# Kernel tuning notes

Hardware: AMD Instinct MI355X
Metric: run time of the kernel (lower is better)

## Reference

```python
import jax, jax.numpy as jnp
import numpy as np

BS, QLEN, DIM, NH = 2, 2048, 1024, 16
HD = DIM // NH


def setup_inputs() -> dict:
    key = jax.random.key(0)
    ks = jax.random.split(key, 6)
    std = 0.02
    return {
        "x": jax.random.normal(ks[0], (BS, QLEN, DIM), dtype=jnp.float32),
        "mask": jnp.ones((BS, QLEN), dtype=jnp.float32),
        "Wq": jax.random.normal(ks[1], (DIM, DIM), dtype=jnp.float32) * std,
        "bq": jnp.zeros((DIM,), dtype=jnp.float32),
        "Wk": jax.random.normal(ks[2], (DIM, DIM), dtype=jnp.float32) * std,
        "bk": jnp.zeros((DIM,), dtype=jnp.float32),
        "Wv": jax.random.normal(ks[3], (DIM, DIM), dtype=jnp.float32) * std,
        "bv": jnp.zeros((DIM,), dtype=jnp.float32),
        "Wo": jax.random.normal(ks[4], (DIM, DIM), dtype=jnp.float32) * std,
        "bo": jnp.zeros((DIM,), dtype=jnp.float32),
    }


def reference(x, mask, Wq, bq, Wk, bk, Wv, bv, Wo, bo):
    bs, qlen, dim = x.shape
    # project and split heads: [bs, nh, len, hd]
    def split_heads(t):
        return t.reshape(bs, -1, NH, HD).transpose(0, 2, 1, 3)

    q = split_heads(x @ Wq + bq) / jnp.sqrt(jnp.float32(HD))
    k = split_heads(x @ Wk + bk)
    v = split_heads(x @ Wv + bv)

    scores = jnp.einsum("bhqd,bhkd->bhqk", q, k)  # [bs, nh, qlen, klen]
    m = mask.reshape(bs, 1, 1, -1)  # 2D mask -> broadcast over heads and q
    scores = scores - 1e30 * (1.0 - m)
    weights = jax.nn.softmax(scores, axis=-1)
    # dropout p=0.0 at inference -> no-op; head_mask is None
    context = jnp.einsum("bhqk,bhkd->bhqd", weights, v)
    context = context.transpose(0, 2, 1, 3).reshape(bs, qlen, NH * HD)
    return context @ Wo + bo
```

## Files before the change

kernel.cpp:

```cpp
#include <hip/hip_runtime.h>
#include <stdint.h>

#define BSZ  2
#define SEQ  2048
#define DIM  1024
#define NHD  16
#define HD   64
#define MTOT (BSZ*SEQ)

using short8  = __attribute__((ext_vector_type(8))) short;
using floatx4 = __attribute__((ext_vector_type(4))) float;

#define QSCALE 0.18033688011112042f
#define BIGM   1.44e30f

__device__ __forceinline__ unsigned short f2bf(float f) {
    unsigned int u = __float_as_uint(f);
    u += 0x7fffu + ((u >> 16) & 1u);
    return (unsigned short)(u >> 16);
}
__device__ __forceinline__ unsigned int pk2r(float a, float b) {
    unsigned int ua = __float_as_uint(a) + 0x8000u;
    unsigned int ub = __float_as_uint(b) + 0x8000u;
    return __builtin_amdgcn_perm(ub, ua, 0x07060302);
}

__device__ __forceinline__ void gll16(const void* g, const void* lds) {
    unsigned int loff = (unsigned int)(unsigned long long)lds;
    __builtin_amdgcn_global_load_lds(
        (const __attribute__((address_space(1))) unsigned int*)g,
        (__attribute__((address_space(3))) unsigned int*)loff, 16, 0, 0);
}

__global__ __launch_bounds__(256)
void conv_x(const float* __restrict__ X, unsigned short* __restrict__ Xbf) {
    size_t i = ((size_t)blockIdx.x * 256 + threadIdx.x) * 8;
    float4 a = *(const float4*)(X + i);
    float4 b = *(const float4*)(X + i + 4);
    uint4 u = {pk2r(a.x, a.y), pk2r(a.z, a.w), pk2r(b.x, b.y), pk2r(b.z, b.w)};
    *(uint4*)(Xbf + i) = u;
}

__global__ __launch_bounds__(256)
void conv_wt(const float* __restrict__ Wq, const float* __restrict__ Wk,
             const float* __restrict__ Wv, const float* __restrict__ Wo,
             unsigned short* __restrict__ Wt3, unsigned short* __restrict__ Wto)
{
    __shared__ float tile[64 * 65];
    const int z = blockIdx.z;
    const float* W = (z == 0) ? Wq : (z == 1) ? Wk : (z == 2) ? Wv : Wo;
    unsigned short* out = (z < 3) ? (Wt3 + (size_t)z * DIM * DIM) : Wto;
    const int k0 = blockIdx.x * 64, n0 = blockIdx.y * 64;
    const int t = threadIdx.x;
    const int r = t >> 2, c0 = (t & 3) * 16;
#pragma unroll
    for (int j = 0; j < 4; ++j) {
        float4 v = *(const float4*)&W[(size_t)(k0 + r) * DIM + n0 + c0 + j * 4];
        tile[r * 65 + c0 + j * 4 + 0] = v.x;
        tile[r * 65 + c0 + j * 4 + 1] = v.y;
        tile[r * 65 + c0 + j * 4 + 2] = v.z;
        tile[r * 65 + c0 + j * 4 + 3] = v.w;
    }
    __syncthreads();
    unsigned int p[8];
#pragma unroll
    for (int j = 0; j < 8; ++j)
        p[j] = pk2r(tile[(c0 + 2 * j) * 65 + r], tile[(c0 + 2 * j + 1) * 65 + r]);
    uint4 u0 = {p[0], p[1], p[2], p[3]}, u1 = {p[4], p[5], p[6], p[7]};
    unsigned short* dst = out + (size_t)(n0 + r) * DIM + k0 + c0;
    *(uint4*)dst = u0;
    *(uint4*)(dst + 8) = u1;
}

__global__ __launch_bounds__(256)
void qkv_gemm(const unsigned short* __restrict__ Xbf,
              const unsigned short* __restrict__ Wt3,
              const float* __restrict__ bq, const float* __restrict__ bk,
              const float* __restrict__ bv,
              unsigned short* __restrict__ Qb,
              unsigned short* __restrict__ Kb,
              unsigned short* __restrict__ VbT)
{
    __shared__ unsigned short As[128 * 32];
    __shared__ unsigned short Bs[128 * 32];

    const int t = threadIdx.x, w = t >> 6, lane = t & 63;
    const int lm = lane & 15, grp = lane >> 4;
    const int wm = w >> 1, wn = w & 1;
    const int m0 = blockIdx.x * 128;
    const int mat = blockIdx.y >> 3;
    const int n0 = (blockIdx.y & 7) * 128;
    const unsigned short* Bg = Wt3 + (size_t)mat * DIM * DIM;

    const int lr = lane >> 2, lc = (lane & 3) * 8;

    floatx4 acc[4][4];
#pragma unroll
    for (int i = 0; i < 4; ++i)
#pragma unroll
        for (int j = 0; j < 4; ++j) acc[i][j] = (floatx4){0.f, 0.f, 0.f, 0.f};

    for (int kt = 0; kt < DIM / 32; ++kt) {
        const int k0 = kt * 32;
        const int r0 = w * 16;
        gll16(Xbf + (size_t)(m0 + r0 + lr) * DIM + k0 + lc,      &As[r0 * 32]);
        gll16(Xbf + (size_t)(m0 + 64 + r0 + lr) * DIM + k0 + lc, &As[(64 + r0) * 32]);
        gll16(Bg  + (size_t)(n0 + r0 + lr) * DIM + k0 + lc,      &Bs[r0 * 32]);
        gll16(Bg  + (size_t)(n0 + 64 + r0 + lr) * DIM + k0 + lc, &Bs[(64 + r0) * 32]);
        __syncthreads();
        short8 af[4], bf[4];
#pragma unroll
        for (int mt = 0; mt < 4; ++mt)
            af[mt] = *(const short8*)&As[(wm * 64 + mt * 16 + lm) * 32 + grp * 8];
#pragma unroll
        for (int nt = 0; nt < 4; ++nt)
            bf[nt] = *(const short8*)&Bs[(wn * 64 + nt * 16 + lm) * 32 + grp * 8];
#pragma unroll
        for (int mt = 0; mt < 4; ++mt)
#pragma unroll
            for (int nt = 0; nt < 4; ++nt)
                acc[mt][nt] = __builtin_amdgcn_mfma_f32_16x16x32_bf16(af[mt], bf[nt], acc[mt][nt], 0, 0, 0);
        __syncthreads();
    }

    if (mat == 2) {
#pragma unroll
        for (int nt = 0; nt < 4; ++nt) {
            const int c = n0 + wn * 64 + nt * 16 + lm;
            const float bb = bv[c];
            const int h = c >> 6, d = c & 63;
#pragma unroll
            for (int mt = 0; mt < 4; ++mt) {
                const int r = m0 + wm * 64 + mt * 16 + grp * 4;
                const int b = r >> 11, s = r & 2047;
                const int si = s & 63, sb = s & ~63;
                const int cg = si >> 4, g = (si >> 2) & 3;
                const int unit = (((cg & 1) << 2) | g) ^ (d & 7);
                const int sph = sb + unit * 8 + ((cg >> 1) << 2);
                uint2 pv;
                pv.x = pk2r(acc[mt][nt][0] + bb, acc[mt][nt][1] + bb);
                pv.y = pk2r(acc[mt][nt][2] + bb, acc[mt][nt][3] + bb);
                *(uint2*)&VbT[(((size_t)(b * NHD + h)) * HD + d) * SEQ + sph] = pv;
            }
        }
    } else if (mat == 1) {
#pragma unroll
        for (int nt = 0; nt < 4; ++nt) {
            const int c = n0 + wn * 64 + nt * 16 + lm;
            const float bb = bk[c];
            const int h = c >> 6, d = c & 63;
#pragma unroll
            for (int mt = 0; mt < 4; ++mt)
#pragma unroll
                for (int reg = 0; reg < 4; ++reg) {
                    const int r = m0 + wm * 64 + mt * 16 + grp * 4 + reg;
                    const int b = r >> 11, s = r & 2047;
                    const int dphys = (((d >> 3) ^ (s & 7)) << 3) | (d & 7);
                    Kb[(((size_t)(b * NHD + h)) * SEQ + s) * HD + dphys] =
                        f2bf(acc[mt][nt][reg] + bb);
                }
        }
    } else {
#pragma unroll
        for (int nt = 0; nt < 4; ++nt) {
            const int c = n0 + wn * 64 + nt * 16 + lm;
            const float bb = bq[c];
            const int h = c >> 6, d = c & 63;
#pragma unroll
            for (int mt = 0; mt < 4; ++mt)
#pragma unroll
                for (int reg = 0; reg < 4; ++reg) {
                    const int r = m0 + wm * 64 + mt * 16 + grp * 4 + reg;
                    const int b = r >> 11, s = r & 2047;
                    Qb[(((size_t)(b * NHD + h)) * SEQ + s) * HD + d] =
                        f2bf((acc[mt][nt][reg] + bb) * QSCALE);
                }
        }
    }
}

__global__ __launch_bounds__(256, 4)
void attn(const unsigned short* __restrict__ Qb,
          const unsigned short* __restrict__ Kb,
          const unsigned short* __restrict__ VbT,
          const float* __restrict__ mask,
          unsigned short* __restrict__ Cb)
{
    __shared__ unsigned short Kt[2][64 * 64];
    __shared__ unsigned short Vt[2][64 * 64];
    __shared__ float Msk[SEQ];

    const int t = threadIdx.x, w = t >> 6, lane = t & 63;
    const int lm = lane & 15, grp = lane >> 4;
    const int x7 = lm & 7;
    const int bh = blockIdx.y, b = bh >> 4, h = bh & 15;
    const int q0 = blockIdx.x * 64;

    short8 qf[2];
    {
        const unsigned short* qrow = Qb + ((size_t)bh * SEQ + q0 + w * 16 + lm) * HD;
        qf[0] = *(const short8*)(qrow + grp * 8);
        qf[1] = *(const short8*)(qrow + 32 + grp * 8);
    }

    {
        const float* mb = mask + b * SEQ;
        const int i = t * 8;
        float4 a = *(const float4*)(mb + i);
        float4 c = *(const float4*)(mb + i + 4);
        float4 ra = {__builtin_fmaf(a.x, BIGM, -BIGM), __builtin_fmaf(a.y, BIGM, -BIGM),
                     __builtin_fmaf(a.z, BIGM, -BIGM), __builtin_fmaf(a.w, BIGM, -BIGM)};
        float4 rc = {__builtin_fmaf(c.x, BIGM, -BIGM), __builtin_fmaf(c.y, BIGM, -BIGM),
                     __builtin_fmaf(c.z, BIGM, -BIGM), __builtin_fmaf(c.w, BIGM, -BIGM)};
        *(float4*)&Msk[i]     = ra;
        *(float4*)&Msk[i + 4] = rc;
    }

    floatx4 oacc[4];
#pragma unroll
    for (int i = 0; i < 4; ++i) oacc[i] = (floatx4){0.f, 0.f, 0.f, 0.f};
    float lpart = 0.f;

    const unsigned short* Kg = Kb + (size_t)bh * SEQ * HD;
    const unsigned short* Vg = VbT + (size_t)bh * HD * SEQ;
    const int srow = lane >> 3, scol = (lane & 7) * 8;

    gll16(Kg + (size_t)(w * 16 + srow) * HD + scol,      &Kt[0][(w * 16) * 64]);
    gll16(Kg + (size_t)(w * 16 + 8 + srow) * HD + scol,  &Kt[0][(w * 16 + 8) * 64]);
    gll16(Vg + (size_t)(w * 16 + srow) * SEQ + scol,     &Vt[0][(w * 16) * 64]);
    gll16(Vg + (size_t)(w * 16 + 8 + srow) * SEQ + scol, &Vt[0][(w * 16 + 8) * 64]);

#pragma unroll 1
    for (int kt = 0; kt < SEQ / 64; ++kt) {
        const int cur = kt & 1;
        const int kb = kt * 64;
        __syncthreads();
        if (kt + 1 < SEQ / 64) {
            const int nxt = cur ^ 1, kn = (kt + 1) * 64;
            gll16(Kg + (size_t)(kn + w * 16 + srow) * HD + scol,      &Kt[nxt][(w * 16) * 64]);
            gll16(Kg + (size_t)(kn + w * 16 + 8 + srow) * HD + scol,  &Kt[nxt][(w * 16 + 8) * 64]);
            gll16(Vg + (size_t)(w * 16 + srow) * SEQ + kn + scol,     &Vt[nxt][(w * 16) * 64]);
            gll16(Vg + (size_t)(w * 16 + 8 + srow) * SEQ + kn + scol, &Vt[nxt][(w * 16 + 8) * 64]);
        }

        floatx4 sv[4];
#pragma unroll
        for (int cg = 0; cg < 4; ++cg) {
            short8 a0 = *(const short8*)&Kt[cur][(cg * 16 + lm) * 64 + ((grp    ) ^ x7) * 8];
            short8 a1 = *(const short8*)&Kt[cur][(cg * 16 + lm) * 64 + ((4 + grp) ^ x7) * 8];
            floatx4 s = (floatx4){0.f, 0.f, 0.f, 0.f};
            s = __builtin_amdgcn_mfma_f32_16x16x32_bf16(a0, qf[0], s, 0, 0, 0);
            s = __builtin_amdgcn_mfma_f32_16x16x32_bf16(a1, qf[1], s, 0, 0, 0);
            sv[cg] = s;
        }

        short8 vf[4][2];
#pragma unroll
        for (int dg = 0; dg < 4; ++dg) {
            vf[dg][0] = *(const short8*)&Vt[cur][(dg * 16 + lm) * 64 + ((grp    ) ^ x7) * 8];
            vf[dg][1] = *(const short8*)&Vt[cur][(dg * 16 + lm) * 64 + ((4 + grp) ^ x7) * 8];
        }

        float p[4][4];
#pragma unroll
        for (int cg = 0; cg < 4; ++cg) {
            float4 md = *(const float4*)&Msk[kb + cg * 16 + grp * 4];
            p[cg][0] = __builtin_exp2f(sv[cg][0] + md.x);
            p[cg][1] = __builtin_exp2f(sv[cg][1] + md.y);
            p[cg][2] = __builtin_exp2f(sv[cg][2] + md.z);
            p[cg][3] = __builtin_exp2f(sv[cg][3] + md.w);
            lpart += (p[cg][0] + p[cg][1]) + (p[cg][2] + p[cg][3]);
        }

        uint4 u0, u1;
        u0.x = pk2r(p[0][0], p[0][1]); u0.y = pk2r(p[0][2], p[0][3]);
        u0.z = pk2r(p[2][0], p[2][1]); u0.w = pk2r(p[2][2], p[2][3]);
        u1.x = pk2r(p[1][0], p[1][1]); u1.y = pk2r(p[1][2], p[1][3]);
        u1.z = pk2r(p[3][0], p[3][1]); u1.w = pk2r(p[3][2], p[3][3]);
        short8 ap0 = *(const short8*)&u0;
        short8 ap1 = *(const short8*)&u1;

#pragma unroll
        for (int dg = 0; dg < 4; ++dg) {
            oacc[dg] = __builtin_amdgcn_mfma_f32_16x16x32_bf16(ap0, vf[dg][0], oacc[dg], 0, 0, 0);
            oacc[dg] = __builtin_amdgcn_mfma_f32_16x16x32_bf16(ap1, vf[dg][1], oacc[dg], 0, 0, 0);
        }
    }

    lpart += __shfl_xor(lpart, 16);
    lpart += __shfl_xor(lpart, 32);
    const float linv = (lpart > 0.f) ? 1.0f / lpart : 0.f;
    float inv[4];
#pragma unroll
    for (int r = 0; r < 4; ++r) inv[r] = __shfl(linv, grp * 4 + r);
#pragma unroll
    for (int dg = 0; dg < 4; ++dg)
#pragma unroll
        for (int r = 0; r < 4; ++r) {
            const int s = q0 + w * 16 + grp * 4 + r;
            Cb[((size_t)(b * SEQ + s)) * DIM + h * HD + dg * 16 + lm] =
                f2bf(oacc[dg][r] * inv[r]);
        }
}

__global__ __launch_bounds__(256)
void out_gemm(const unsigned short* __restrict__ Cb,
              const unsigned short* __restrict__ Wto,
              const float* __restrict__ bo,
              float* __restrict__ out)
{
    __shared__ unsigned short As[128 * 32];
    __shared__ unsigned short Bs[64 * 32];

    const int t = threadIdx.x, w = t >> 6, lane = t & 63;
    const int lm = lane & 15, grp = lane >> 4;
    const int m0 = blockIdx.x * 128;
    const int n0 = blockIdx.y * 64;

    const int lr = lane >> 2, lc = (lane & 3) * 8;

    floatx4 acc[2][4];
#pragma unroll
    for (int i = 0; i < 2; ++i)
#pragma unroll
        for (int j = 0; j < 4; ++j) acc[i][j] = (floatx4){0.f, 0.f, 0.f, 0.f};

    for (int kt = 0; kt < DIM / 32; ++kt) {
        const int k0 = kt * 32;
        const int r0 = w * 16;
        gll16(Cb  + (size_t)(m0 + r0 + lr) * DIM + k0 + lc,      &As[r0 * 32]);
        gll16(Cb  + (size_t)(m0 + 64 + r0 + lr) * DIM + k0 + lc, &As[(64 + r0) * 32]);
        gll16(Wto + (size_t)(n0 + r0 + lr) * DIM + k0 + lc,      &Bs[r0 * 32]);
        __syncthreads();
        short8 af[2], bf[4];
#pragma unroll
        for (int mt = 0; mt < 2; ++mt)
            af[mt] = *(const short8*)&As[(w * 32 + mt * 16 + lm) * 32 + grp * 8];
#pragma unroll
        for (int nt = 0; nt < 4; ++nt)
            bf[nt] = *(const short8*)&Bs[(nt * 16 + lm) * 32 + grp * 8];
#pragma unroll
        for (int mt = 0; mt < 2; ++mt)
#pragma unroll
            for (int nt = 0; nt < 4; ++nt)
                acc[mt][nt] = __builtin_amdgcn_mfma_f32_16x16x32_bf16(af[mt], bf[nt], acc[mt][nt], 0, 0, 0);
        __syncthreads();
    }

#pragma unroll
    for (int nt = 0; nt < 4; ++nt) {
        const int c = n0 + nt * 16 + lm;
        const float bb = bo[c];
#pragma unroll
        for (int mt = 0; mt < 2; ++mt)
#pragma unroll
            for (int reg = 0; reg < 4; ++reg) {
                const int r = m0 + w * 32 + mt * 16 + grp * 4 + reg;
                out[(size_t)r * DIM + c] = acc[mt][nt][reg] + bb;
            }
    }
}

extern "C" void kernel_launch(void* const* d_in, const int* in_sizes, int n_in,
                              void* d_out, int out_size, void* d_ws, size_t ws_size,
                              hipStream_t stream)
{
    const float* x    = (const float*)d_in[0];
    const float* mask = (const float*)d_in[1];
    const float* Wq   = (const float*)d_in[2];
    const float* bq   = (const float*)d_in[3];
    const float* Wk   = (const float*)d_in[4];
    const float* bk   = (const float*)d_in[5];
    const float* Wv   = (const float*)d_in[6];
    const float* bv   = (const float*)d_in[7];
    const float* Wo   = (const float*)d_in[8];
    const float* bo   = (const float*)d_in[9];
    float* out = (float*)d_out;

    const size_t M1 = (size_t)DIM * DIM;
    unsigned short* Qb  = (unsigned short*)d_ws;
    unsigned short* Kb  = Qb  + 4 * M1;
    unsigned short* VbT = Kb  + 4 * M1;
    unsigned short* Cb  = VbT + 4 * M1;
    unsigned short* Xbf = Cb  + 4 * M1;
    unsigned short* Wt3 = Xbf + 4 * M1;
    unsigned short* Wto = Wt3 + 3 * M1;

    conv_x <<<dim3((MTOT * DIM) / 2048), 256, 0, stream>>>(x, Xbf);
    conv_wt<<<dim3(16, 16, 4), 256, 0, stream>>>(Wq, Wk, Wv, Wo, Wt3, Wto);
    qkv_gemm<<<dim3(MTOT / 128, 24), 256, 0, stream>>>(Xbf, Wt3, bq, bk, bv, Qb, Kb, VbT);
    attn<<<dim3(SEQ / 64, BSZ * NHD), 256, 0, stream>>>(Qb, Kb, VbT, mask, Cb);
    out_gemm<<<dim3(MTOT / 128, DIM / 64), 256, 0, stream>>>(Cb, Wto, bo, out);
}
```

Before: 218.1 us.

## Double-buffer GEMM tiles, swap MFMA operands for vector stores, precompute mask penalty

```diff
diff --git a/kernel.cpp b/kernel.cpp
--- a/kernel.cpp
+++ b/kernel.cpp
@@ -13,6 +13,7 @@
 
 #define QSCALE 0.18033688011112042f
 #define BIGM   1.44e30f
+#define NXB    ((MTOT * DIM) / 2048)
 
 __device__ __forceinline__ unsigned short f2bf(float f) {
     unsigned int u = __float_as_uint(f);
@@ -33,7 +34,22 @@
 }
 
 __global__ __launch_bounds__(256)
-void conv_x(const float* __restrict__ X, unsigned short* __restrict__ Xbf) {
+void conv_x(const float* __restrict__ X, unsigned short* __restrict__ Xbf,
+            const float* __restrict__ mask, float* __restrict__ Pen) {
+    if (blockIdx.x >= NXB) {
+        const int bb = blockIdx.x - NXB;
+        const int i = threadIdx.x * 8;
+        const float* mb = mask + bb * SEQ;
+        float4 a = *(const float4*)(mb + i);
+        float4 c = *(const float4*)(mb + i + 4);
+        float4 ra = {__builtin_fmaf(a.x, BIGM, -BIGM), __builtin_fmaf(a.y, BIGM, -BIGM),
+                     __builtin_fmaf(a.z, BIGM, -BIGM), __builtin_fmaf(a.w, BIGM, -BIGM)};
+        float4 rc = {__builtin_fmaf(c.x, BIGM, -BIGM), __builtin_fmaf(c.y, BIGM, -BIGM),
+                     __builtin_fmaf(c.z, BIGM, -BIGM), __builtin_fmaf(c.w, BIGM, -BIGM)};
+        *(float4*)&Pen[bb * SEQ + i]     = ra;
+        *(float4*)&Pen[bb * SEQ + i + 4] = rc;
+        return;
+    }
     size_t i = ((size_t)blockIdx.x * 256 + threadIdx.x) * 8;
     float4 a = *(const float4*)(X + i);
     float4 b = *(const float4*)(X + i + 4);
@@ -81,8 +97,8 @@
               unsigned short* __restrict__ Kb,
               unsigned short* __restrict__ VbT)
 {
-    __shared__ unsigned short As[128 * 32];
-    __shared__ unsigned short Bs[128 * 32];
+    __shared__ unsigned short As[2][128 * 32];
+    __shared__ unsigned short Bs[2][128 * 32];
 
     const int t = threadIdx.x, w = t >> 6, lane = t & 63;
     const int lm = lane & 15, grp = lane >> 4;
@@ -91,8 +107,8 @@
     const int mat = blockIdx.y >> 3;
     const int n0 = (blockIdx.y & 7) * 128;
     const unsigned short* Bg = Wt3 + (size_t)mat * DIM * DIM;
-
     const int lr = lane >> 2, lc = (lane & 3) * 8;
+    const int r0 = w * 16;
 
     floatx4 acc[4][4];
 #pragma unroll
@@ -100,28 +116,43 @@
 #pragma unroll
         for (int j = 0; j < 4; ++j) acc[i][j] = (floatx4){0.f, 0.f, 0.f, 0.f};
 
+#define QKV_STAGE(KT, BUF) do {                                                   \
+        const int k0_ = (KT) * 32;                                                \
+        gll16(Xbf + (size_t)(m0 + r0 + lr) * DIM + k0_ + lc,      &As[BUF][r0 * 32]);        \
+        gll16(Xbf + (size_t)(m0 + 64 + r0 + lr) * DIM + k0_ + lc, &As[BUF][(64 + r0) * 32]); \
+        gll16(Bg  + (size_t)(n0 + r0 + lr) * DIM + k0_ + lc,      &Bs[BUF][r0 * 32]);        \
+        gll16(Bg  + (size_t)(n0 + 64 + r0 + lr) * DIM + k0_ + lc, &Bs[BUF][(64 + r0) * 32]); \
+    } while (0)
+
+    QKV_STAGE(0, 0);
+
+#pragma unroll 1
     for (int kt = 0; kt < DIM / 32; ++kt) {
-        const int k0 = kt * 32;
-        const int r0 = w * 16;
-        gll16(Xbf + (size_t)(m0 + r0 + lr) * DIM + k0 + lc,      &As[r0 * 32]);
-        gll16(Xbf + (size_t)(m0 + 64 + r0 + lr) * DIM + k0 + lc, &As[(64 + r0) * 32]);
-        gll16(Bg  + (size_t)(n0 + r0 + lr) * DIM + k0 + lc,      &Bs[r0 * 32]);
-        gll16(Bg  + (size_t)(n0 + 64 + r0 + lr) * DIM + k0 + lc, &Bs[(64 + r0) * 32]);
+        const int cur = kt & 1;
         __syncthreads();
+        if (kt + 1 < DIM / 32) QKV_STAGE(kt + 1, cur ^ 1);
         short8 af[4], bf[4];
 #pragma unroll
         for (int mt = 0; mt < 4; ++mt)
-            af[mt] = *(const short8*)&As[(wm * 64 + mt * 16 + lm) * 32 + grp * 8];
+            af[mt] = *(const short8*)&As[cur][(wm * 64 + mt * 16 + lm) * 32 + grp * 8];
 #pragma unroll
         for (int nt = 0; nt < 4; ++nt)
-            bf[nt] = *(const short8*)&Bs[(wn * 64 + nt * 16 + lm) * 32 + grp * 8];
-#pragma unroll
-        for (int mt = 0; mt < 4; ++mt)
-#pragma unroll
-            for (int nt = 0; nt < 4; ++nt)
-                acc[mt][nt] = __builtin_amdgcn_mfma_f32_16x16x32_bf16(af[mt], bf[nt], acc[mt][nt], 0, 0, 0);
-        __syncthreads();
-    }
+            bf[nt] = *(const short8*)&Bs[cur][(wn * 64 + nt * 16 + lm) * 32 + grp * 8];
+        if (mat != 2) {
+#pragma unroll
+            for (int mt = 0; mt < 4; ++mt)
+#pragma unroll
+                for (int nt = 0; nt < 4; ++nt)
+                    acc[mt][nt] = __builtin_amdgcn_mfma_f32_16x16x32_bf16(bf[nt], af[mt], acc[mt][nt], 0, 0, 0);
+        } else {
+#pragma unroll
+            for (int mt = 0; mt < 4; ++mt)
+#pragma unroll
+                for (int nt = 0; nt < 4; ++nt)
+                    acc[mt][nt] = __builtin_amdgcn_mfma_f32_16x16x32_bf16(af[mt], bf[nt], acc[mt][nt], 0, 0, 0);
+        }
+    }
+#undef QKV_STAGE
 
     if (mat == 2) {
 #pragma unroll
@@ -143,38 +174,26 @@
                 *(uint2*)&VbT[(((size_t)(b * NHD + h)) * HD + d) * SEQ + sph] = pv;
             }
         }
-    } else if (mat == 1) {
+    } else {
+        const float* bias = (mat == 0) ? bq : bk;
+        unsigned short* dst = (mat == 0) ? Qb : Kb;
+        const float sc = (mat == 0) ? QSCALE : 1.0f;
 #pragma unroll
         for (int nt = 0; nt < 4; ++nt) {
-            const int c = n0 + wn * 64 + nt * 16 + lm;
-            const float bb = bk[c];
-            const int h = c >> 6, d = c & 63;
-#pragma unroll
-            for (int mt = 0; mt < 4; ++mt)
-#pragma unroll
-                for (int reg = 0; reg < 4; ++reg) {
-                    const int r = m0 + wm * 64 + mt * 16 + grp * 4 + reg;
-                    const int b = r >> 11, s = r & 2047;
-                    const int dphys = (((d >> 3) ^ (s & 7)) << 3) | (d & 7);
-                    Kb[(((size_t)(b * NHD + h)) * SEQ + s) * HD + dphys] =
-                        f2bf(acc[mt][nt][reg] + bb);
-                }
-        }
-    } else {
-#pragma unroll
-        for (int nt = 0; nt < 4; ++nt) {
-            const int c = n0 + wn * 64 + nt * 16 + lm;
-            const float bb = bq[c];
-            const int h = c >> 6, d = c & 63;
-#pragma unroll
-            for (int mt = 0; mt < 4; ++mt)
-#pragma unroll
-                for (int reg = 0; reg < 4; ++reg) {
-                    const int r = m0 + wm * 64 + mt * 16 + grp * 4 + reg;
-                    const int b = r >> 11, s = r & 2047;
-                    Qb[(((size_t)(b * NHD + h)) * SEQ + s) * HD + d] =
-                        f2bf((acc[mt][nt][reg] + bb) * QSCALE);
-                }
+            const int c0 = n0 + wn * 64 + nt * 16 + grp * 4;
+            float4 bb = *(const float4*)&bias[c0];
+            const int h = c0 >> 6, d0 = c0 & 63;
+#pragma unroll
+            for (int mt = 0; mt < 4; ++mt) {
+                const int r = m0 + wm * 64 + mt * 16 + lm;
+                const int b = r >> 11, s = r & 2047;
+                uint2 pv;
+                pv.x = pk2r((acc[mt][nt][0] + bb.x) * sc, (acc[mt][nt][1] + bb.y) * sc);
+                pv.y = pk2r((acc[mt][nt][2] + bb.z) * sc, (acc[mt][nt][3] + bb.w) * sc);
+                const int dd = (mat == 0) ? d0
+                             : ((((d0 >> 3) ^ (s & 7)) << 3) | (d0 & 7));
+                *(uint2*)&dst[(((size_t)(b * NHD + h)) * SEQ + s) * HD + dd] = pv;
+            }
         }
     }
 }
@@ -183,12 +202,11 @@
 void attn(const unsigned short* __restrict__ Qb,
           const unsigned short* __restrict__ Kb,
           const unsigned short* __restrict__ VbT,
-          const float* __restrict__ mask,
+          const float* __restrict__ Pen,
           unsigned short* __restrict__ Cb)
 {
     __shared__ unsigned short Kt[2][64 * 64];
     __shared__ unsigned short Vt[2][64 * 64];
-    __shared__ float Msk[SEQ];
 
     const int t = threadIdx.x, w = t >> 6, lane = t & 63;
     const int lm = lane & 15, grp = lane >> 4;
@@ -203,19 +221,6 @@
         qf[1] = *(const short8*)(qrow + 32 + grp * 8);
     }
 
-    {
-        const float* mb = mask + b * SEQ;
-        const int i = t * 8;
-        float4 a = *(const float4*)(mb + i);
-        float4 c = *(const float4*)(mb + i + 4);
-        float4 ra = {__builtin_fmaf(a.x, BIGM, -BIGM), __builtin_fmaf(a.y, BIGM, -BIGM),
-                     __builtin_fmaf(a.z, BIGM, -BIGM), __builtin_fmaf(a.w, BIGM, -BIGM)};
-        float4 rc = {__builtin_fmaf(c.x, BIGM, -BIGM), __builtin_fmaf(c.y, BIGM, -BIGM),
-                     __builtin_fmaf(c.z, BIGM, -BIGM), __builtin_fmaf(c.w, BIGM, -BIGM)};
-        *(float4*)&Msk[i]     = ra;
-        *(float4*)&Msk[i + 4] = rc;
-    }
-
     floatx4 oacc[4];
 #pragma unroll
     for (int i = 0; i < 4; ++i) oacc[i] = (floatx4){0.f, 0.f, 0.f, 0.f};
@@ -223,6 +228,7 @@
 
     const unsigned short* Kg = Kb + (size_t)bh * SEQ * HD;
     const unsigned short* Vg = VbT + (size_t)bh * HD * SEQ;
+    const float* Pb = Pen + b * SEQ;
     const int srow = lane >> 3, scol = (lane & 7) * 8;
 
     gll16(Kg + (size_t)(w * 16 + srow) * HD + scol,      &Kt[0][(w * 16) * 64]);
@@ -235,6 +241,12 @@
         const int cur = kt & 1;
         const int kb = kt * 64;
         __syncthreads();
+
+        float4 md[4];
+#pragma unroll
+        for (int cg = 0; cg < 4; ++cg)
+            md[cg] = *(const float4*)&Pb[kb + cg * 16 + grp * 4];
+
         if (kt + 1 < SEQ / 64) {
             const int nxt = cur ^ 1, kn = (kt + 1) * 64;
             gll16(Kg + (size_t)(kn + w * 16 + srow) * HD + scol,      &Kt[nxt][(w * 16) * 64]);
@@ -264,11 +276,10 @@
         float p[4][4];
 #pragma unroll
         for (int cg = 0; cg < 4; ++cg) {
-            float4 md = *(const float4*)&Msk[kb + cg * 16 + grp * 4];
-            p[cg][0] = __builtin_exp2f(sv[cg][0] + md.x);
-            p[cg][1] = __builtin_exp2f(sv[cg][1] + md.y);
-            p[cg][2] = __builtin_exp2f(sv[cg][2] + md.z);
-            p[cg][3] = __builtin_exp2f(sv[cg][3] + md.w);
+            p[cg][0] = __builtin_exp2f(sv[cg][0] + md[cg].x);
+            p[cg][1] = __builtin_exp2f(sv[cg][1] + md[cg].y);
+            p[cg][2] = __builtin_exp2f(sv[cg][2] + md[cg].z);
+            p[cg][3] = __builtin_exp2f(sv[cg][3] + md[cg].w);
             lpart += (p[cg][0] + p[cg][1]) + (p[cg][2] + p[cg][3]);
         }
 
@@ -309,15 +320,15 @@
               const float* __restrict__ bo,
               float* __restrict__ out)
 {
-    __shared__ unsigned short As[128 * 32];
-    __shared__ unsigned short Bs[64 * 32];
+    __shared__ unsigned short As[2][128 * 32];
+    __shared__ unsigned short Bs[2][64 * 32];
 
     const int t = threadIdx.x, w = t >> 6, lane = t & 63;
     const int lm = lane & 15, grp = lane >> 4;
     const int m0 = blockIdx.x * 128;
     const int n0 = blockIdx.y * 64;
-
     const int lr = lane >> 2, lc = (lane & 3) * 8;
+    const int r0 = w * 16;
 
     floatx4 acc[2][4];
 #pragma unroll
@@ -325,39 +336,46 @@
 #pragma unroll
         for (int j = 0; j < 4; ++j) acc[i][j] = (floatx4){0.f, 0.f, 0.f, 0.f};
 
+#define OUT_STAGE(KT, BUF) do {                                                   \
+        const int k0_ = (KT) * 32;                                                \
+        gll16(Cb  + (size_t)(m0 + r0 + lr) * DIM + k0_ + lc,      &As[BUF][r0 * 32]);        \
+        gll16(Cb  + (size_t)(m0 + 64 + r0 + lr) * DIM + k0_ + lc, &As[BUF][(64 + r0) * 32]); \
+        gll16(Wto + (size_t)(n0 + r0 + lr) * DIM + k0_ + lc,      &Bs[BUF][r0 * 32]);        \
+    } while (0)
+
+    OUT_STAGE(0, 0);
+
+#pragma unroll 1
     for (int kt = 0; kt < DIM / 32; ++kt) {
-        const int k0 = kt * 32;
-        const int r0 = w * 16;
-        gll16(Cb  + (size_t)(m0 + r0 + lr) * DIM + k0 + lc,      &As[r0 * 32]);
-        gll16(Cb  + (size_t)(m0 + 64 + r0 + lr) * DIM + k0 + lc, &As[(64 + r0) * 32]);
-        gll16(Wto + (size_t)(n0 + r0 + lr) * DIM + k0 + lc,      &Bs[r0 * 32]);
+        const int cur = kt & 1;
         __syncthreads();
+        if (kt + 1 < DIM / 32) OUT_STAGE(kt + 1, cur ^ 1);
         short8 af[2], bf[4];
 #pragma unroll
         for (int mt = 0; mt < 2; ++mt)
-            af[mt] = *(const short8*)&As[(w * 32 + mt * 16 + lm) * 32 + grp * 8];
+            af[mt] = *(const short8*)&As[cur][(w * 32 + mt * 16 + lm) * 32 + grp * 8];
 #pragma unroll
         for (int nt = 0; nt < 4; ++nt)
-            bf[nt] = *(const short8*)&Bs[(nt * 16 + lm) * 32 + grp * 8];
+            bf[nt] = *(const short8*)&Bs[cur][(nt * 16 + lm) * 32 + grp * 8];
 #pragma unroll
         for (int mt = 0; mt < 2; ++mt)
 #pragma unroll
             for (int nt = 0; nt < 4; ++nt)
-                acc[mt][nt] = __builtin_amdgcn_mfma_f32_16x16x32_bf16(af[mt], bf[nt], acc[mt][nt], 0, 0, 0);
-        __syncthreads();
-    }
+                acc[mt][nt] = __builtin_amdgcn_mfma_f32_16x16x32_bf16(bf[nt], af[mt], acc[mt][nt], 0, 0, 0);
+    }
+#undef OUT_STAGE
 
 #pragma unroll
     for (int nt = 0; nt < 4; ++nt) {
-        const int c = n0 + nt * 16 + lm;
-        const float bb = bo[c];
-#pragma unroll
-        for (int mt = 0; mt < 2; ++mt)
-#pragma unroll
-            for (int reg = 0; reg < 4; ++reg) {
-                const int r = m0 + w * 32 + mt * 16 + grp * 4 + reg;
-                out[(size_t)r * DIM + c] = acc[mt][nt][reg] + bb;
-            }
+        const int c0 = n0 + nt * 16 + grp * 4;
+        float4 bb = *(const float4*)&bo[c0];
+#pragma unroll
+        for (int mt = 0; mt < 2; ++mt) {
+            const int r = m0 + w * 32 + mt * 16 + lm;
+            float4 o = {acc[mt][nt][0] + bb.x, acc[mt][nt][1] + bb.y,
+                        acc[mt][nt][2] + bb.z, acc[mt][nt][3] + bb.w};
+            *(float4*)&out[(size_t)r * DIM + c0] = o;
+        }
     }
 }
 
@@ -385,10 +403,11 @@
     unsigned short* Xbf = Cb  + 4 * M1;
     unsigned short* Wt3 = Xbf + 4 * M1;
     unsigned short* Wto = Wt3 + 3 * M1;
-
-    conv_x <<<dim3((MTOT * DIM) / 2048), 256, 0, stream>>>(x, Xbf);
+    float*          Pen = (float*)(Wto + M1);
+
+    conv_x <<<dim3(NXB + BSZ), 256, 0, stream>>>(x, Xbf, mask, Pen);
     conv_wt<<<dim3(16, 16, 4), 256, 0, stream>>>(Wq, Wk, Wv, Wo, Wt3, Wto);
     qkv_gemm<<<dim3(MTOT / 128, 24), 256, 0, stream>>>(Xbf, Wt3, bq, bk, bv, Qb, Kb, VbT);
-    attn<<<dim3(SEQ / 64, BSZ * NHD), 256, 0, stream>>>(Qb, Kb, VbT, mask, Cb);
+    attn<<<dim3(SEQ / 64, BSZ * NHD), 256, 0, stream>>>(Qb, Kb, VbT, Pen, Cb);
     out_gemm<<<dim3(MTOT / 128, DIM / 64), 256, 0, stream>>>(Cb, Wto, bo, out);
 }
```

Result: no change. 218.4 us (+0.2%).
